# Kernel tuning notes

Hardware: AMD Instinct MI355X
Metric: run time of the kernel (lower is better)

The kernel has to match this reference:

```python
import jax, jax.numpy as jnp
import numpy as np
import math

INPUT_DIM = 1024
EXPANSION = 4
SPARSITY = 0.15
ACT_SPARSITY = 0.1
OUTPUT_DIM = INPUT_DIM * EXPANSION
K = max(1, int(OUTPUT_DIM * ACT_SPARSITY))  # 409
BATCH = 16384


def setup_inputs() -> dict:
    key = jax.random.key(0)
    kx, kw, km = jax.random.split(key, 3)
    x = jax.random.normal(kx, (BATCH, INPUT_DIM), dtype=jnp.float32)
    # sparse random projection buffer, built exactly as in __init__
    w = jax.random.normal(kw, (OUTPUT_DIM, INPUT_DIM), dtype=jnp.float32)
    mask = (jax.random.uniform(km, (OUTPUT_DIM, INPUT_DIM)) < SPARSITY).astype(jnp.float32)
    scale = 1.5 / math.sqrt(INPUT_DIM * SPARSITY)
    projection_weights = w * mask * scale
    return {"x": x, "projection_weights": projection_weights}


def reference(x, projection_weights):
    # data-dependent bipolar rescale: torch uses `if x.min() >= 0`; express with where
    x_bipolar = jnp.where(x.min() >= 0, (x - 0.5) * 2.0, x)
    # [B, D_out] dense projection
    projected = jnp.einsum("bi,oi->bo", x_bipolar, projection_weights)
    # k-WTA: threshold at k-th largest value per row
    top_values, _ = jax.lax.top_k(projected, K)
    threshold = top_values[:, -1:]  # [B, 1]
    mask = (projected >= threshold).astype(projected.dtype)
    encoded = jax.nn.relu(projected) * mask
    # F.normalize(p=2, dim=1): divide by max(norm, eps)
    norm = jnp.sqrt(jnp.sum(encoded * encoded, axis=1, keepdims=True))
    return encoded / jnp.maximum(norm, 1e-12)
```

## Files before the change

### kernel.cpp

```cpp
#include <hip/hip_runtime.h>

#define BATCH   16384
#define IN_DIM  1024
#define OUT_DIM 4096
#define K_TOP   409
#define DELTA_W 6.5e-3f

typedef _Float16 half8  __attribute__((ext_vector_type(8)));
typedef _Float16 half4v __attribute__((ext_vector_type(4)));
typedef float    f32x4  __attribute__((ext_vector_type(4)));

#define WS_XH_OFF   256
#define WS_WH_OFF   (WS_XH_OFF + (size_t)BATCH * IN_DIM * 2)
#define WS_WV_OFF   (WS_WH_OFF + (size_t)OUT_DIM * IN_DIM * 2)
#define WS_WI_OFF   (WS_WV_OFF + (size_t)OUT_DIM * 256 * 4)
#define WS_WN_OFF   (WS_WI_OFF + (size_t)OUT_DIM * 256 * 2)
#define WS_NEEDED   (WS_WV_OFF)
#define WS_NEED3    (WS_WN_OFF + (size_t)OUT_DIM * 4)


__global__ __launch_bounds__(256)
void k_hasneg(const float* __restrict__ x, int n, int* __restrict__ flag) {
    const int stride = gridDim.x * blockDim.x;
    bool neg = false;
    for (int i = blockIdx.x * blockDim.x + threadIdx.x; i < n; i += stride)
        neg |= (x[i] < 0.0f);
    unsigned long long b = __ballot(neg);
    if (b != 0ULL && (threadIdx.x & 63) == 0)
        atomicOr(flag, 1);
}

__global__ __launch_bounds__(256)
void k_cvt2(const float* __restrict__ x, const float* __restrict__ w,
            _Float16* __restrict__ xh, _Float16* __restrict__ wh,
            float* __restrict__ wv, unsigned short* __restrict__ wi,
            int* __restrict__ wn, int use_csr, const int* __restrict__ flag) {
    const bool bipolar = (*flag == 0);
    const int tid = threadIdx.x;
    const int lane = tid & 63;
    const int wrow = blockIdx.x * 4 + (tid >> 6);

    const float* wr = w + (size_t)wrow * IN_DIM;
    const float4* wr4 = (const float4*)(wr + lane * 16);
    _Float16* whr = wh + (size_t)wrow * IN_DIM + lane * 16;
    float4 v[4];
    int cnt = 0;
    #pragma unroll
    for (int q = 0; q < 4; ++q) {
        v[q] = wr4[q];
        ((half4v*)whr)[q] = half4v{ (_Float16)v[q].x, (_Float16)v[q].y,
                                    (_Float16)v[q].z, (_Float16)v[q].w };
        cnt += (v[q].x != 0.0f) + (v[q].y != 0.0f)
             + (v[q].z != 0.0f) + (v[q].w != 0.0f);
    }
    if (use_csr) {
        int off = cnt;
        #pragma unroll
        for (int d = 1; d < 64; d <<= 1) {
            int t = __shfl_up(off, d);
            if (lane >= d) off += t;
        }
        const int total = __shfl(off, 63);
        off -= cnt;
        float* dv = wv + (size_t)wrow * 256;
        unsigned short* di = wi + (size_t)wrow * 256;
        int pos = off;
        #pragma unroll
        for (int q = 0; q < 4; ++q) {
            #pragma unroll
            for (int e = 0; e < 4; ++e) {
                float f = (e == 0) ? v[q].x : (e == 1) ? v[q].y
                        : (e == 2) ? v[q].z : v[q].w;
                if (f != 0.0f) {
                    dv[pos] = f;
                    di[pos] = (unsigned short)(lane * 16 + q * 4 + e);
                    ++pos;
                }
            }
        }
        if (lane == 0) {
            const int n4 = (total + 3) & ~3;
            for (int i = total; i < n4 && i < 256; ++i) { dv[i] = 0.0f; di[i] = 0; }
            wn[wrow] = total;
        }
    }

    const float4* x4 = (const float4*)x;
    half4v* xh4 = (half4v*)xh;
    const int base = blockIdx.x * 4096;
    #pragma unroll
    for (int u = 0; u < 16; ++u) {
        const int idx = base + u * 256 + tid;
        float4 xv = x4[idx];
        if (bipolar) {
            xv.x = (xv.x - 0.5f) * 2.0f; xv.y = (xv.y - 0.5f) * 2.0f;
            xv.z = (xv.z - 0.5f) * 2.0f; xv.w = (xv.w - 0.5f) * 2.0f;
        }
        xh4[idx] = half4v{ (_Float16)xv.x, (_Float16)xv.y,
                           (_Float16)xv.z, (_Float16)xv.w };
    }
}

__global__ __launch_bounds__(512, 2)
void k_gemm16(const _Float16* __restrict__ xh, const _Float16* __restrict__ wh,
              float* __restrict__ out) {
    __shared__ _Float16 Ah[2][256 * 64];
    __shared__ _Float16 Bh[2][256 * 64];
    const int tid = threadIdx.x;
    const int bm = blockIdx.x, bn = blockIdx.y;
    const int lane = tid & 63;
    const int wv = tid >> 6;
    const int wm = wv >> 2, wn = wv & 3;
    const int lr = lane & 15, lk = lane >> 4;

    const int srow = (lane >> 3);
    const int sslot = (lane & 7) ^ srow;
    f32x4 acc[8][4] = {};

    const _Float16* aS[4]; const _Float16* bS[4];
    int dOff[4];
    #pragma unroll
    for (int i = 0; i < 4; ++i) {
        const int rb = i * 64 + wv * 8;
        aS[i] = xh + (size_t)(bm * 256 + rb + srow) * IN_DIM + sslot * 8;
        bS[i] = wh + (size_t)(bn * 256 + rb + srow) * IN_DIM + sslot * 8;
        dOff[i] = rb * 64;
    }

    #pragma unroll
    for (int i = 0; i < 4; ++i) {
        __builtin_amdgcn_global_load_lds((const __attribute__((address_space(1))) void*)(aS[i]), (__attribute__((address_space(3))) void*)&Ah[0][dOff[i]], 16, 0, 0);
        __builtin_amdgcn_global_load_lds((const __attribute__((address_space(1))) void*)(bS[i]), (__attribute__((address_space(3))) void*)&Bh[0][dOff[i]], 16, 0, 0);
    }
    __syncthreads();

    int cur = 0;
    #pragma unroll 1
    for (int t = 0; t < 16; ++t) {
        if (t < 15) {
            const int kt = (t + 1) * 64;
            #pragma unroll
            for (int i = 0; i < 4; ++i) {
                __builtin_amdgcn_global_load_lds((const __attribute__((address_space(1))) void*)(aS[i] + kt), (__attribute__((address_space(3))) void*)&Ah[cur ^ 1][dOff[i]], 16, 0, 0);
                __builtin_amdgcn_global_load_lds((const __attribute__((address_space(1))) void*)(bS[i] + kt), (__attribute__((address_space(3))) void*)&Bh[cur ^ 1][dOff[i]], 16, 0, 0);
            }
        }
        #pragma unroll
        for (int h = 0; h < 2; ++h) {
            half8 bf[4];
            #pragma unroll
            for (int j = 0; j < 4; ++j) {
                const int rbv = wn * 64 + j * 16 + lr;
                const int sb = (h * 4 + lk) ^ (rbv & 7);
                bf[j] = *(const half8*)&Bh[cur][rbv * 64 + (sb << 3)];
            }
            #pragma unroll
            for (int hf = 0; hf < 2; ++hf) {
                half8 af[4];
                #pragma unroll
                for (int i = 0; i < 4; ++i) {
                    const int ra = wm * 128 + (hf * 4 + i) * 16 + lr;
                    const int sa = (h * 4 + lk) ^ (ra & 7);
                    af[i] = *(const half8*)&Ah[cur][ra * 64 + (sa << 3)];
                }
                #pragma unroll
                for (int i = 0; i < 4; ++i)
                    #pragma unroll
                    for (int j = 0; j < 4; ++j)
                        acc[hf * 4 + i][j] = __builtin_amdgcn_mfma_f32_16x16x32_f16(
                            af[i], bf[j], acc[hf * 4 + i][j], 0, 0, 0);
            }
        }
        __syncthreads();
        cur ^= 1;
    }
    #pragma unroll
    for (int i = 0; i < 8; ++i)
        #pragma unroll
        for (int j = 0; j < 4; ++j)
            #pragma unroll
            for (int q = 0; q < 4; ++q) {
                const int row = bm * 256 + wm * 128 + i * 16 + lk * 4 + q;
                const int col = bn * 256 + wn * 64 + j * 16 + lr;
                _Float16* fo = (_Float16*)((char*)out + (size_t)row * OUT_DIM * 4);
                fo[col] = (_Float16)acc[i][j][q];
            }
}

__global__ __launch_bounds__(256)
void k_self(float* __restrict__ po, const float* __restrict__ x,
            const float* __restrict__ wvals, const unsigned short* __restrict__ widx,
            const int* __restrict__ wn, const float* __restrict__ wfull,
            int use_csr, const int* __restrict__ flag) {
    __shared__ unsigned int bins[256];
    __shared__ float fred[4];
    __shared__ unsigned int wsum[4];
    __shared__ int ired[4];
    __shared__ int s_b, s_b2;
    __shared__ unsigned int s_slot, s_hi1;
    __shared__ int bcol[64];
    __shared__ float bnp[64];
    __shared__ unsigned char bsel[64];
    __shared__ float xs[IN_DIM];

    const int row = blockIdx.x;
    const int tid = threadIdx.x;
    const int lane = tid & 63, wq = tid >> 6;
    const _Float16* fr = (const _Float16*)((const char*)po + (size_t)row * OUT_DIM * 4);

    half8 h0 = *(const half8*)&fr[tid * 8];
    half8 h1 = *(const half8*)&fr[2048 + tid * 8];
    float fv[16];
    float vmax = -1e30f;
    #pragma unroll
    for (int e = 0; e < 8; ++e) {
        fv[e] = (float)h0[e];
        fv[8 + e] = (float)h1[e];
        vmax = fmaxf(vmax, fmaxf(fv[e], fv[8 + e]));
    }
    #pragma unroll
    for (int off = 32; off > 0; off >>= 1)
        vmax = fmaxf(vmax, __shfl_xor(vmax, off));
    if (lane == 0) fred[wq] = vmax;
    bins[tid] = 0;
    if (tid == 0) { s_slot = 0; s_b = 0; s_b2 = 0; s_hi1 = 0; }
    __syncthreads();
    vmax = fmaxf(fmaxf(fmaxf(fred[0], fred[1]), fmaxf(fred[2], fred[3])), 1e-6f);
    const float scale1 = 256.0f / vmax;
    const float invscale1 = vmax * (1.0f / 256.0f);

    #pragma unroll
    for (int e = 0; e < 16; ++e) {
        float f = fv[e];
        if (f > 0.0f) {
            int b = (int)(f * scale1);
            if (b > 255) b = 255;
            atomicAdd(&bins[b], 1u);
        }
    }
    __syncthreads();
    {
        const unsigned int c = bins[255 - tid];
        unsigned int sc = c;
        #pragma unroll
        for (int off = 1; off < 64; off <<= 1) {
            unsigned int t2 = __shfl_up(sc, off);
            if (lane >= off) sc += t2;
        }
        if (lane == 63) wsum[wq] = sc;
        __syncthreads();
        for (int q = 0; q < wq; ++q) sc += wsum[q];
        if ((int)sc >= K_TOP && (int)(sc - c) < K_TOP) {
            s_b = 255 - tid;
            s_hi1 = sc - c;
        }
    }
    __syncthreads();
    const int b1 = s_b;
    const unsigned int hi1 = s_hi1;
    const float blo = (float)b1 * invscale1;
    const float scale2 = scale1 * 256.0f;
    const float s2w = invscale1 * (1.0f / 256.0f);

    bins[tid] = 0;
    __syncthreads();
    #pragma unroll
    for (int e = 0; e < 16; ++e) {
        float f = fv[e];
        if (f > 0.0f) {
            int b = (int)(f * scale1);
            if (b > 255) b = 255;
            if (b == b1) {
                int b2 = (int)((f - blo) * scale2);
                if (b2 < 0) b2 = 0;
                if (b2 > 255) b2 = 255;
                atomicAdd(&bins[b2], 1u);
            }
        }
    }
    __syncthreads();
    {
        const unsigned int c = bins[255 - tid];
        unsigned int sc = c;
        #pragma unroll
        for (int off = 1; off < 64; off <<= 1) {
            unsigned int t2 = __shfl_up(sc, off);
            if (lane >= off) sc += t2;
        }
        if (lane == 63) wsum[wq] = sc;
        __syncthreads();
        for (int q = 0; q < wq; ++q) sc += wsum[q];
        if ((int)(hi1 + sc) >= K_TOP && (int)(hi1 + sc - c) < K_TOP)
            s_b2 = 255 - tid;
    }
    __syncthreads();
    const float thi = blo + (float)(s_b2 + 1) * s2w + DELTA_W;
    const float tlo = blo + (float)s_b2 * s2w - DELTA_W;

    int hic = 0;
    #pragma unroll
    for (int e = 0; e < 16; ++e) {
        float f = fv[e];
        if (f > thi) ++hic;
        else if (f >= tlo) {
            unsigned int p = atomicAdd(&s_slot, 1u);
            const int j = (e < 8) ? (tid * 8 + e) : (2048 + tid * 8 + e - 8);
            if (p < 64) bcol[p] = j;
        }
    }
    #pragma unroll
    for (int off = 32; off > 0; off >>= 1)
        hic += __shfl_xor(hic, off);
    if (lane == 0) ired[wq] = hic;
    __syncthreads();
    const int hi = ired[0] + ired[1] + ired[2] + ired[3];
    const int nb = (int)s_slot;
    const int nbc = nb > 64 ? 64 : nb;
    int krem = K_TOP - hi; if (krem > nb) krem = nb; if (krem < 0) krem = 0;
    const bool need = (nb != krem);

    if (need) {
        const bool bipolar = (*flag == 0);
        float4 xv = ((const float4*)(x + (size_t)row * IN_DIM))[tid];
        if (bipolar) {
            xv.x = __fmul_rn(__fadd_rn(xv.x, -0.5f), 2.0f);
            xv.y = __fmul_rn(__fadd_rn(xv.y, -0.5f), 2.0f);
            xv.z = __fmul_rn(__fadd_rn(xv.z, -0.5f), 2.0f);
            xv.w = __fmul_rn(__fadd_rn(xv.w, -0.5f), 2.0f);
        }
        ((float4*)xs)[tid] = xv;
        __syncthreads();
        if (tid < nbc) {
            const int col = bcol[tid];
            float p = 0.0f;
            if (use_csr) {
                const int n4 = (wn[col] + 3) >> 2;
                const float4* v4 = (const float4*)(wvals + (size_t)col * 256);
                const ushort4* i4 = (const ushort4*)(widx + (size_t)col * 256);
                #pragma unroll 2
                for (int i = 0; i < n4; ++i) {
                    float4 vv = v4[i];
                    ushort4 ii = i4[i];
                    p = __fmaf_rn(xs[ii.x], vv.x, p);
                    p = __fmaf_rn(xs[ii.y], vv.y, p);
                    p = __fmaf_rn(xs[ii.z], vv.z, p);
                    p = __fmaf_rn(xs[ii.w], vv.w, p);
                }
            } else {
                const float4* wr4 = (const float4*)(wfull + (size_t)col * IN_DIM);
                const float4* xs4 = (const float4*)xs;
                #pragma unroll 4
                for (int i = 0; i < IN_DIM / 4; ++i) {
                    float4 xq = xs4[i];
                    float4 wq2 = wr4[i];
                    p = __fmaf_rn(xq.x, wq2.x, p);
                    p = __fmaf_rn(xq.y, wq2.y, p);
                    p = __fmaf_rn(xq.z, wq2.z, p);
                    p = __fmaf_rn(xq.w, wq2.w, p);
                }
            }
            bnp[tid] = p;
        }
        __syncthreads();
        if (tid < nbc) {
            const float v = bnp[tid];
            int gc = 0;
            for (int l = 0; l < nbc; ++l) gc += (bnp[l] > v);
            bsel[tid] = (gc < krem) ? 1 : 0;
        }
        __syncthreads();
    }

    float ov[16];
    float nrm2 = 0.0f;
    #pragma unroll
    for (int e = 0; e < 16; ++e) {
        float f = fv[e];
        const int j = (e < 8) ? (tid * 8 + e) : (2048 + tid * 8 + e - 8);
        bool sel = (f > thi);
        float val = f;
        if (!sel && f >= tlo) {
            if (!need) sel = true;
            else {
                for (int m = 0; m < nbc; ++m)
                    if (bcol[m] == j) {
                        sel = (bsel[m] != 0);
                        val = bnp[m];
                        break;
                    }
            }
        }
        float eo = (sel && val > 0.0f) ? val : 0.0f;
        ov[e] = eo;
        nrm2 += eo * eo;
    }
    #pragma unroll
    for (int off = 32; off > 0; off >>= 1)
        nrm2 += __shfl_xor(nrm2, off);
    if (lane == 0) fred[wq] = nrm2;
    __syncthreads();
    const float total = fred[0] + fred[1] + fred[2] + fred[3];
    const float inv = 1.0f / fmaxf(sqrtf(total), 1e-12f);

    float4* p4 = (float4*)(po + (size_t)row * OUT_DIM);
    #pragma unroll
    for (int h = 0; h < 2; ++h) {
        const int base = (h == 0) ? 0 : 8;
        const int fi = (h == 0) ? (tid * 2) : (512 + tid * 2);
        float4 o0 = make_float4(ov[base + 0] * inv, ov[base + 1] * inv,
                                ov[base + 2] * inv, ov[base + 3] * inv);
        float4 o1 = make_float4(ov[base + 4] * inv, ov[base + 5] * inv,
                                ov[base + 6] * inv, ov[base + 7] * inv);
        p4[fi] = o0;
        p4[fi + 1] = o1;
    }
}

extern "C" void kernel_launch(void* const* d_in, const int* in_sizes, int n_in,
                              void* d_out, int out_size, void* d_ws, size_t ws_size,
                              hipStream_t stream) {
    const float* x = (const float*)d_in[0];
    const float* w = (const float*)d_in[1];
    float* out = (float*)d_out;
    int* flag = (int*)d_ws;
    const int use_csr = (ws_size >= WS_NEED3) ? 1 : 0;

    hipMemsetAsync(flag, 0, sizeof(int), stream);
    k_hasneg<<<2048, 256, 0, stream>>>(x, BATCH * IN_DIM, flag);

    _Float16* xh = (_Float16*)((char*)d_ws + WS_XH_OFF);
    _Float16* wh = (_Float16*)((char*)d_ws + WS_WH_OFF);
    float* wv = (float*)((char*)d_ws + WS_WV_OFF);
    unsigned short* wi = (unsigned short*)((char*)d_ws + WS_WI_OFF);
    int* wn = (int*)((char*)d_ws + WS_WN_OFF);

    k_cvt2<<<OUT_DIM / 4, 256, 0, stream>>>(x, w, xh, wh, wv, wi, wn,
                                            use_csr, flag);
    dim3 g(BATCH / 256, OUT_DIM / 256);
    k_gemm16<<<g, 512, 0, stream>>>(xh, wh, out);

    k_self<<<BATCH, 256, 0, stream>>>(out, x, wv, wi, wn, w, use_csr, flag);
}
```

Before: 438.3 us.

## Use 512 threads per row in k-WTA kernel with cached bins and nontemporal stores

```diff
diff --git a/kernel.cpp b/kernel.cpp
--- a/kernel.cpp
+++ b/kernel.cpp
@@ -187,15 +187,15 @@
             }
 }
 
-__global__ __launch_bounds__(256)
+__global__ __launch_bounds__(512)
 void k_self(float* __restrict__ po, const float* __restrict__ x,
             const float* __restrict__ wvals, const unsigned short* __restrict__ widx,
             const int* __restrict__ wn, const float* __restrict__ wfull,
             int use_csr, const int* __restrict__ flag) {
     __shared__ unsigned int bins[256];
-    __shared__ float fred[4];
+    __shared__ float fred[8];
     __shared__ unsigned int wsum[4];
-    __shared__ int ired[4];
+    __shared__ int ired[8];
     __shared__ int s_b, s_b2;
     __shared__ unsigned int s_slot, s_hi1;
     __shared__ int bcol[64];
@@ -208,119 +208,8 @@
     const int lane = tid & 63, wq = tid >> 6;
     const _Float16* fr = (const _Float16*)((const char*)po + (size_t)row * OUT_DIM * 4);
 
-    half8 h0 = *(const half8*)&fr[tid * 8];
-    half8 h1 = *(const half8*)&fr[2048 + tid * 8];
-    float fv[16];
-    float vmax = -1e30f;
-    #pragma unroll
-    for (int e = 0; e < 8; ++e) {
-        fv[e] = (float)h0[e];
-        fv[8 + e] = (float)h1[e];
-        vmax = fmaxf(vmax, fmaxf(fv[e], fv[8 + e]));
-    }
-    #pragma unroll
-    for (int off = 32; off > 0; off >>= 1)
-        vmax = fmaxf(vmax, __shfl_xor(vmax, off));
-    if (lane == 0) fred[wq] = vmax;
-    bins[tid] = 0;
-    if (tid == 0) { s_slot = 0; s_b = 0; s_b2 = 0; s_hi1 = 0; }
-    __syncthreads();
-    vmax = fmaxf(fmaxf(fmaxf(fred[0], fred[1]), fmaxf(fred[2], fred[3])), 1e-6f);
-    const float scale1 = 256.0f / vmax;
-    const float invscale1 = vmax * (1.0f / 256.0f);
-
-    #pragma unroll
-    for (int e = 0; e < 16; ++e) {
-        float f = fv[e];
-        if (f > 0.0f) {
-            int b = (int)(f * scale1);
-            if (b > 255) b = 255;
-            atomicAdd(&bins[b], 1u);
-        }
-    }
-    __syncthreads();
-    {
-        const unsigned int c = bins[255 - tid];
-        unsigned int sc = c;
-        #pragma unroll
-        for (int off = 1; off < 64; off <<= 1) {
-            unsigned int t2 = __shfl_up(sc, off);
-            if (lane >= off) sc += t2;
-        }
-        if (lane == 63) wsum[wq] = sc;
-        __syncthreads();
-        for (int q = 0; q < wq; ++q) sc += wsum[q];
-        if ((int)sc >= K_TOP && (int)(sc - c) < K_TOP) {
-            s_b = 255 - tid;
-            s_hi1 = sc - c;
-        }
-    }
-    __syncthreads();
-    const int b1 = s_b;
-    const unsigned int hi1 = s_hi1;
-    const float blo = (float)b1 * invscale1;
-    const float scale2 = scale1 * 256.0f;
-    const float s2w = invscale1 * (1.0f / 256.0f);
-
-    bins[tid] = 0;
-    __syncthreads();
-    #pragma unroll
-    for (int e = 0; e < 16; ++e) {
-        float f = fv[e];
-        if (f > 0.0f) {
-            int b = (int)(f * scale1);
-            if (b > 255) b = 255;
-            if (b == b1) {
-                int b2 = (int)((f - blo) * scale2);
-                if (b2 < 0) b2 = 0;
-                if (b2 > 255) b2 = 255;
-                atomicAdd(&bins[b2], 1u);
-            }
-        }
-    }
-    __syncthreads();
-    {
-        const unsigned int c = bins[255 - tid];
-        unsigned int sc = c;
-        #pragma unroll
-        for (int off = 1; off < 64; off <<= 1) {
-            unsigned int t2 = __shfl_up(sc, off);
-            if (lane >= off) sc += t2;
-        }
-        if (lane == 63) wsum[wq] = sc;
-        __syncthreads();
-        for (int q = 0; q < wq; ++q) sc += wsum[q];
-        if ((int)(hi1 + sc) >= K_TOP && (int)(hi1 + sc - c) < K_TOP)
-            s_b2 = 255 - tid;
-    }
-    __syncthreads();
-    const float thi = blo + (float)(s_b2 + 1) * s2w + DELTA_W;
-    const float tlo = blo + (float)s_b2 * s2w - DELTA_W;
-
-    int hic = 0;
-    #pragma unroll
-    for (int e = 0; e < 16; ++e) {
-        float f = fv[e];
-        if (f > thi) ++hic;
-        else if (f >= tlo) {
-            unsigned int p = atomicAdd(&s_slot, 1u);
-            const int j = (e < 8) ? (tid * 8 + e) : (2048 + tid * 8 + e - 8);
-            if (p < 64) bcol[p] = j;
-        }
-    }
-    #pragma unroll
-    for (int off = 32; off > 0; off >>= 1)
-        hic += __shfl_xor(hic, off);
-    if (lane == 0) ired[wq] = hic;
-    __syncthreads();
-    const int hi = ired[0] + ired[1] + ired[2] + ired[3];
-    const int nb = (int)s_slot;
-    const int nbc = nb > 64 ? 64 : nb;
-    int krem = K_TOP - hi; if (krem > nb) krem = nb; if (krem < 0) krem = 0;
-    const bool need = (nb != krem);
-
-    if (need) {
-        const bool bipolar = (*flag == 0);
+    const bool bipolar = (*flag == 0);
+    if (tid < 256) {
         float4 xv = ((const float4*)(x + (size_t)row * IN_DIM))[tid];
         if (bipolar) {
             xv.x = __fmul_rn(__fadd_rn(xv.x, -0.5f), 2.0f);
@@ -329,7 +218,130 @@
             xv.w = __fmul_rn(__fadd_rn(xv.w, -0.5f), 2.0f);
         }
         ((float4*)xs)[tid] = xv;
+    }
+
+    half8 h0 = *(const half8*)&fr[tid * 8];
+    float fv[8];
+    int bb[8];
+    float vmax = -1e30f;
+    #pragma unroll
+    for (int e = 0; e < 8; ++e) {
+        fv[e] = (float)h0[e];
+        vmax = fmaxf(vmax, fv[e]);
+    }
+    #pragma unroll
+    for (int off = 32; off > 0; off >>= 1)
+        vmax = fmaxf(vmax, __shfl_xor(vmax, off));
+    if (lane == 0) fred[wq] = vmax;
+    if (tid < 256) bins[tid] = 0;
+    if (tid == 0) { s_slot = 0; s_b = 0; s_b2 = 0; s_hi1 = 0; }
+    __syncthreads();
+    vmax = fred[0];
+    #pragma unroll
+    for (int q = 1; q < 8; ++q) vmax = fmaxf(vmax, fred[q]);
+    vmax = fmaxf(vmax, 1e-6f);
+    const float scale1 = 256.0f / vmax;
+    const float invscale1 = vmax * (1.0f / 256.0f);
+
+    #pragma unroll
+    for (int e = 0; e < 8; ++e) {
+        float f = fv[e];
+        int b = -1;
+        if (f > 0.0f) {
+            b = (int)(f * scale1);
+            if (b > 255) b = 255;
+            atomicAdd(&bins[b], 1u);
+        }
+        bb[e] = b;
+    }
+    __syncthreads();
+    {
+        unsigned int c = 0, sc = 0;
+        if (tid < 256) {
+            c = bins[255 - tid];
+            sc = c;
+            #pragma unroll
+            for (int off = 1; off < 64; off <<= 1) {
+                unsigned int t2 = __shfl_up(sc, off);
+                if (lane >= off) sc += t2;
+            }
+            if (lane == 63) wsum[wq] = sc;
+        }
         __syncthreads();
+        if (tid < 256) {
+            for (int q = 0; q < wq; ++q) sc += wsum[q];
+            if ((int)sc >= K_TOP && (int)(sc - c) < K_TOP) {
+                s_b = 255 - tid;
+                s_hi1 = sc - c;
+            }
+        }
+    }
+    __syncthreads();
+    const int b1 = s_b;
+    const unsigned int hi1 = s_hi1;
+    const float blo = (float)b1 * invscale1;
+    const float scale2 = scale1 * 256.0f;
+    const float s2w = invscale1 * (1.0f / 256.0f);
+
+    if (tid < 256) bins[tid] = 0;
+    __syncthreads();
+    #pragma unroll
+    for (int e = 0; e < 8; ++e) {
+        if (bb[e] == b1) {
+            int b2 = (int)((fv[e] - blo) * scale2);
+            if (b2 < 0) b2 = 0;
+            if (b2 > 255) b2 = 255;
+            atomicAdd(&bins[b2], 1u);
+        }
+    }
+    __syncthreads();
+    {
+        unsigned int c = 0, sc = 0;
+        if (tid < 256) {
+            c = bins[255 - tid];
+            sc = c;
+            #pragma unroll
+            for (int off = 1; off < 64; off <<= 1) {
+                unsigned int t2 = __shfl_up(sc, off);
+                if (lane >= off) sc += t2;
+            }
+            if (lane == 63) wsum[wq] = sc;
+        }
+        __syncthreads();
+        if (tid < 256) {
+            for (int q = 0; q < wq; ++q) sc += wsum[q];
+            if ((int)(hi1 + sc) >= K_TOP && (int)(hi1 + sc - c) < K_TOP)
+                s_b2 = 255 - tid;
+        }
+    }
+    __syncthreads();
+    const float thi = blo + (float)(s_b2 + 1) * s2w + DELTA_W;
+    const float tlo = blo + (float)s_b2 * s2w - DELTA_W;
+
+    int hic = 0;
+    #pragma unroll
+    for (int e = 0; e < 8; ++e) {
+        float f = fv[e];
+        if (f > thi) ++hic;
+        else if (f >= tlo) {
+            unsigned int p = atomicAdd(&s_slot, 1u);
+            if (p < 64) bcol[p] = tid * 8 + e;
+        }
+    }
+    #pragma unroll
+    for (int off = 32; off > 0; off >>= 1)
+        hic += __shfl_xor(hic, off);
+    if (lane == 0) ired[wq] = hic;
+    __syncthreads();
+    int hi = ired[0];
+    #pragma unroll
+    for (int q = 1; q < 8; ++q) hi += ired[q];
+    const int nb = (int)s_slot;
+    const int nbc = nb > 64 ? 64 : nb;
+    int krem = K_TOP - hi; if (krem > nb) krem = nb; if (krem < 0) krem = 0;
+    const bool need = (nb != krem);
+
+    if (need) {
         if (tid < nbc) {
             const int col = bcol[tid];
             float p = 0.0f;
@@ -371,12 +383,12 @@
         __syncthreads();
     }
 
-    float ov[16];
+    float ov[8];
     float nrm2 = 0.0f;
     #pragma unroll
-    for (int e = 0; e < 16; ++e) {
+    for (int e = 0; e < 8; ++e) {
         float f = fv[e];
-        const int j = (e < 8) ? (tid * 8 + e) : (2048 + tid * 8 + e - 8);
+        const int j = tid * 8 + e;
         bool sel = (f > thi);
         float val = f;
         if (!sel && f >= tlo) {
@@ -399,21 +411,16 @@
         nrm2 += __shfl_xor(nrm2, off);
     if (lane == 0) fred[wq] = nrm2;
     __syncthreads();
-    const float total = fred[0] + fred[1] + fred[2] + fred[3];
+    float total = fred[0];
+    #pragma unroll
+    for (int q = 1; q < 8; ++q) total += fred[q];
     const float inv = 1.0f / fmaxf(sqrtf(total), 1e-12f);
 
-    float4* p4 = (float4*)(po + (size_t)row * OUT_DIM);
-    #pragma unroll
-    for (int h = 0; h < 2; ++h) {
-        const int base = (h == 0) ? 0 : 8;
-        const int fi = (h == 0) ? (tid * 2) : (512 + tid * 2);
-        float4 o0 = make_float4(ov[base + 0] * inv, ov[base + 1] * inv,
-                                ov[base + 2] * inv, ov[base + 3] * inv);
-        float4 o1 = make_float4(ov[base + 4] * inv, ov[base + 5] * inv,
-                                ov[base + 6] * inv, ov[base + 7] * inv);
-        p4[fi] = o0;
-        p4[fi + 1] = o1;
-    }
+    f32x4* p4 = (f32x4*)(po + (size_t)row * OUT_DIM);
+    f32x4 o0 = { ov[0] * inv, ov[1] * inv, ov[2] * inv, ov[3] * inv };
+    f32x4 o1 = { ov[4] * inv, ov[5] * inv, ov[6] * inv, ov[7] * inv };
+    __builtin_nontemporal_store(o0, &p4[tid * 2]);
+    __builtin_nontemporal_store(o1, &p4[tid * 2 + 1]);
 }
 
 extern "C" void kernel_launch(void* const* d_in, const int* in_sizes, int n_in,
@@ -439,5 +446,5 @@
     dim3 g(BATCH / 256, OUT_DIM / 256);
     k_gemm16<<<g, 512, 0, stream>>>(xh, wh, out);
 
-    k_self<<<BATCH, 256, 0, stream>>>(out, x, wv, wi, wn, w, use_csr, flag);
+    k_self<<<BATCH, 512, 0, stream>>>(out, x, wv, wi, wn, w, use_csr, flag);
 }
```

Measured after the change: 486.5 us. 1.11x slower.
